# Optimization experiments

Measured on AMD Instinct MI355X. Metric: run time of the kernel, lower is better.

Reference implementation:

```python
import jax, jax.numpy as jnp
import numpy as np

B, N, C = 1, 2048, 1024
H, D = 16, 64          # num_heads, head_dim
S = 8                  # number of frames; tokens per frame = N // S
NEG_INF = jnp.float32(-1e30)  # stand-in for -inf, numerically safe under jit


def setup_inputs() -> dict:
    key = jax.random.key(0)
    ks = jax.random.split(key, 8)
    x = jax.random.normal(ks[0], (B, N, C), dtype=jnp.float32)
    # tokens grouped contiguously by frame (sorted frame ids)
    frame_ids = jnp.repeat(jnp.arange(S, dtype=jnp.int32), N // S)
    is_hub = jax.random.bernoulli(ks[1], 0.05, (N,))
    adj = jax.random.bernoulli(ks[2], 0.25, (S, S))
    adj = adj.at[jnp.arange(S), jnp.arange(S)].set(True)  # frames always see self
    frame_bias = jax.random.normal(ks[3], (S, S), dtype=jnp.float32) * 0.1
    Wqkv = jax.random.normal(ks[4], (C, 3 * C), dtype=jnp.float32) * 0.02
    bqkv = jnp.zeros((3 * C,), dtype=jnp.float32)
    Wproj = jax.random.normal(ks[5], (C, C), dtype=jnp.float32) * 0.02
    bproj = jnp.zeros((C,), dtype=jnp.float32)
    return {"x": x, "frame_ids": frame_ids, "is_hub": is_hub, "adj": adj,
            "frame_bias": frame_bias, "Wqkv": Wqkv, "bqkv": bqkv,
            "Wproj": Wproj, "bproj": bproj}


def reference(x, frame_ids, is_hub, adj, frame_bias, Wqkv, bqkv, Wproj, bproj):
    # qkv projection: (B,N,3C) -> (3,B,H,N,D)
    qkv = (x @ Wqkv + bqkv).reshape(B, N, 3, H, D).transpose(2, 0, 3, 1, 4)
    q, k, v = qkv[0], qkv[1], qkv[2]

    # flex_attention: scores scaled by 1/sqrt(D) BEFORE score_mod
    scores = jnp.einsum("bhnd,bhmd->bhnm", q, k) * (D ** -0.5)

    # score_mod, vectorized over all (qi,kj) pairs:
    fi = frame_ids                                   # (N,)
    allow = adj[fi][:, fi]                           # (N,N) frame adjacency per token pair
    diff_frame = fi[:, None] != fi[None, :]
    hub_block = diff_frame & (is_hub[:, None] | is_hub[None, :])
    allow = allow & ~hub_block                       # mask_hub_tokens=True
    bias = frame_bias[fi][:, fi]                     # soft_mask=True: add frame-level bias

    scores = jnp.where(allow, scores + bias, NEG_INF)  # broadcast over (b,h)
    attn = jax.nn.softmax(scores, axis=-1)
    out = jnp.einsum("bhnm,bhmd->bhnd", attn, v)
    out = out.transpose(0, 2, 1, 3).reshape(B, N, C)
    return out @ Wproj + bproj
```

## Files before the change

kernel.cpp:

```cpp
#include <hip/hip_runtime.h>

#define NTOK 2048
#define CDIM 1024
#define NHEAD 16
#define HDIM 64
#define NFRM 8
#define FTOK 256

typedef unsigned short ushort;
typedef unsigned long long u64;
typedef __attribute__((ext_vector_type(8))) short short8;
typedef __attribute__((ext_vector_type(8))) ushort ushort8;
typedef __attribute__((ext_vector_type(4))) ushort ushort4v;
typedef __attribute__((ext_vector_type(4))) float floatx4;

__device__ __forceinline__ ushort f2bf(float f) {
    unsigned int u = __float_as_uint(f);
    return (ushort)((u + 0x7fffu + ((u >> 16) & 1u)) >> 16);
}

__device__ __forceinline__ unsigned int cvt_pk_bf16(float lo, float hi) {
    unsigned int r;
    asm volatile("v_cvt_pk_bf16_f32 %0, %1, %2" : "=v"(r) : "v"(lo), "v"(hi));
    return r;
}

__device__ __forceinline__ void gload_lds16(const void* g, void* l) {
    __builtin_amdgcn_global_load_lds(
        (const __attribute__((address_space(1))) unsigned int*)(uintptr_t)g,
        (__attribute__((address_space(3))) unsigned int*)(unsigned int)(uintptr_t)l,
        16, 0, 0);
}

__global__ __launch_bounds__(256)
void prep_kernel(const float* __restrict__ x, ushort* __restrict__ xb,
                 const float* __restrict__ Wqkv, ushort* __restrict__ wqkvT,
                 const float* __restrict__ Wproj, ushort* __restrict__ wprojT,
                 const int* __restrict__ is_hub, u64* __restrict__ hubmask)
{
    __shared__ ushort LT[64][72];
    const int b = blockIdx.x, t = threadIdx.x;

    if (b < 2048) {
        int i = b * 256 + t;
        float4 f = ((const float4*)x)[i];
        ushort4v o = { f2bf(f.x), f2bf(f.y), f2bf(f.z), f2bf(f.w) };
        ((ushort4v*)xb)[i] = o;
        return;
    }
    if (b >= 3072) {
        if (t < NTOK / 64) {
            u64 m = 0;
            for (int j = 0; j < 64; ++j)
                m |= (u64)(is_hub[t * 64 + j] != 0) << j;
            hubmask[t] = m;
        }
        return;
    }

    const float* W; ushort* WT; int K, N, n0, k0;
    if (b < 2816) { int idx = b - 2048; W = Wqkv;  WT = wqkvT;  K = 1024; N = 3072;
                    n0 = (idx % 48) * 64; k0 = (idx / 48) * 64; }
    else          { int idx = b - 2816; W = Wproj; WT = wprojT; K = 1024; N = 1024;
                    n0 = (idx & 15) * 64; k0 = (idx >> 4) * 64; }

    const int kr = t >> 4, nc = t & 15;
#pragma unroll
    for (int i = 0; i < 4; ++i) {
        int k = kr + i * 16;
        float4 w4 = *(const float4*)(W + (size_t)(k0 + k) * N + n0 + nc * 4);
        LT[nc*4+0][k] = f2bf(w4.x);
        LT[nc*4+1][k] = f2bf(w4.y);
        LT[nc*4+2][k] = f2bf(w4.z);
        LT[nc*4+3][k] = f2bf(w4.w);
    }
    __syncthreads();
    const int n = t >> 2;
#pragma unroll
    for (int half = 0; half < 2; ++half) {
        int kc = (t & 3) + 4 * half;
        ushort8 v = *(const ushort8*)&LT[n][kc * 8];
        *(ushort8*)(WT + (size_t)(n0 + n) * K + k0 + kc * 8) = v;
    }
}

template<int BM>
__global__ __launch_bounds__(256)
void gemm_bt_kernel(const ushort* __restrict__ A, const ushort* __restrict__ BT,
                    const float* __restrict__ bias, void* __restrict__ out,
                    ushort* __restrict__ vtb,
                    int M, int N, int K, int mode)
{
    constexpr int MI = BM / 32;
    __shared__ ushort As[2][BM * 32];
    __shared__ ushort Bs[2][128 * 32];

    const int t = threadIdx.x;
    const int wave = t >> 6, lane = t & 63;
    const int quad = lane >> 4, l15 = lane & 15;
    const int row0 = blockIdx.y * BM, col0 = blockIdx.x * 128;
    const int wm = (wave >> 1) * (BM / 2), wn = (wave & 1) * 64;

    const int sr = lane >> 2;
    const int sc = (lane & 3) * 8;
    const int ra = wave * (BM / 4);
    const int rb = wave * 32;

    floatx4 acc[MI][4];
#pragma unroll
    for (int i = 0; i < MI; ++i)
#pragma unroll
        for (int j = 0; j < 4; ++j) acc[i][j] = (floatx4){0.f, 0.f, 0.f, 0.f};

#pragma unroll
    for (int ii = 0; ii < BM / 64; ++ii)
        gload_lds16(A + (size_t)(row0 + ra + ii * 16 + sr) * K + sc, &As[0][(ra + ii * 16) * 32]);
    gload_lds16(BT + (size_t)(col0 + rb      + sr) * K + sc, &Bs[0][ rb       * 32]);
    gload_lds16(BT + (size_t)(col0 + rb + 16 + sr) * K + sc, &Bs[0][(rb + 16) * 32]);

    const int nk = K >> 5;
    for (int ki = 0; ki < nk; ++ki) {
        __syncthreads();
        if (ki + 1 < nk) {
            const int kn = (ki + 1) << 5;
            const int b = (ki + 1) & 1;
#pragma unroll
            for (int ii = 0; ii < BM / 64; ++ii)
                gload_lds16(A + (size_t)(row0 + ra + ii * 16 + sr) * K + kn + sc, &As[b][(ra + ii * 16) * 32]);
            gload_lds16(BT + (size_t)(col0 + rb      + sr) * K + kn + sc, &Bs[b][ rb       * 32]);
            gload_lds16(BT + (size_t)(col0 + rb + 16 + sr) * K + kn + sc, &Bs[b][(rb + 16) * 32]);
        }
        const ushort* as = As[ki & 1];
        const ushort* bs = Bs[ki & 1];

        short8 af[MI], bfr[4];
#pragma unroll
        for (int i = 0; i < MI; ++i)
            af[i] = *(const short8*)&as[(wm + i * 16 + l15) * 32 + quad * 8];
#pragma unroll
        for (int j = 0; j < 4; ++j)
            bfr[j] = *(const short8*)&bs[(wn + j * 16 + l15) * 32 + quad * 8];
#pragma unroll
        for (int i = 0; i < MI; ++i)
#pragma unroll
            for (int j = 0; j < 4; ++j)
                acc[i][j] = __builtin_amdgcn_mfma_f32_16x16x32_bf16(af[i], bfr[j], acc[i][j], 0, 0, 0);
    }

    if (mode == 0) {
        float* outf = (float*)out;
#pragma unroll
        for (int j = 0; j < 4; ++j) {
            int col = col0 + wn + j * 16 + l15;
            float bb = bias[col];
#pragma unroll
            for (int i = 0; i < MI; ++i) {
                int rowb = row0 + wm + i * 16 + quad * 4;
#pragma unroll
                for (int r = 0; r < 4; ++r)
                    outf[(size_t)(rowb + r) * N + col] = acc[i][j][r] + bb;
            }
        }
    } else {
        ushort* outb = (ushort*)out;
#pragma unroll
        for (int j = 0; j < 4; ++j) {
            int col = col0 + wn + j * 16 + l15;
            float bb = bias[col];
            int part = col >> 10, hh = (col >> 6) & 15, d = col & 63;
            if (part < 2) {
                int half = d >> 5, qk = (d & 31) >> 3, elem = d & 7;
                ushort* base = outb + (size_t)(part * NHEAD + hh) * (NTOK * HDIM);
#pragma unroll
                for (int i = 0; i < MI; ++i) {
                    int rowb = row0 + wm + i * 16 + quad * 4;
#pragma unroll
                    for (int r = 0; r < 4; ++r) {
                        int tok = rowb + r;
                        int tile = tok >> 6, kk = tok & 63;
                        int nt = kk >> 4, lk = kk & 15;
                        base[(size_t)tile * 4096 + ((nt * 2 + half) * 64 + qk * 16 + lk) * 8 + elem]
                            = f2bf(acc[i][j][r] + bb);
                    }
                }
            } else {
                int dt = d >> 4, lv = d & 15;
                ushort* base = vtb + (size_t)hh * (NTOK * HDIM);
#pragma unroll
                for (int i = 0; i < MI; ++i) {
                    int rowb = row0 + wm + i * 16 + quad * 4;
                    int tile = rowb >> 6, kk = rowb & 63;
                    int bslot = ((kk & 15) << 2) | (kk >> 4);
#pragma unroll
                    for (int r = 0; r < 4; ++r) {
                        int s = bslot + 4 * r;
                        int off = ((dt * 2 + (s >> 5)) * 64 + ((s >> 3) & 3) * 16 + lv) * 8 + (s & 7);
                        base[(size_t)tile * 4096 + off] = f2bf(acc[i][j][r] + bb);
                    }
                }
            }
        }
    }
}

__global__ __launch_bounds__(512, 4)
void attn_tile_kernel(const ushort* __restrict__ qkvb,
                      const ushort* __restrict__ vTb,
                      const int* __restrict__ frame_ids,
                      const u64* __restrict__ hubmask,
                      const int* __restrict__ adj,
                      const float* __restrict__ frame_bias,
                      ushort* __restrict__ attnb)
{
    __shared__ ushort Ps[8][16 * 72];
    __shared__ float  Om[4][64][21];

    const int t = threadIdx.x;
    const int wave = t >> 6, lane = t & 63;
    const int wq = wave & 3, wk = wave >> 2;
    const int quad = lane >> 4, l15 = lane & 15;
    const int b = blockIdx.x;
    const int h = b & 15, q0 = (b >> 4) * 64;

    const ushort* Qh = qkvb + (size_t)h * (NTOK * HDIM);
    const ushort* Kh = qkvb + (size_t)(NHEAD + h) * (NTOK * HDIM);
    const ushort* Vh = vTb + (size_t)h * (NTOK * HDIM);

    const ushort* qt = Qh + (size_t)(q0 >> 6) * 4096;
    short8 aq0 = *(const short8*)(qt + ((wq * 2 + 0) * 64 + lane) * 8);
    short8 aq1 = *(const short8*)(qt + ((wq * 2 + 1) * 64 + lane) * 8);

    const int fq = frame_ids[q0];
    unsigned vpack = 0; int nv = 0;
#pragma unroll
    for (int f = 0; f < NFRM; ++f)
        if (adj[fq * NFRM + f]) { vpack |= (unsigned)f << (3 * nv); ++nv; }

    const u64 hmq = hubmask[q0 >> 6];
    int qh[4];
#pragma unroll
    for (int r = 0; r < 4; ++r) qh[r] = (int)((hmq >> (wq * 16 + quad * 4 + r)) & 1);

    float lpart[4] = {0.f, 0.f, 0.f, 0.f};
    floatx4 oacc[4];
#pragma unroll
    for (int dt = 0; dt < 4; ++dt) oacc[dt] = (floatx4){0.f, 0.f, 0.f, 0.f};

    const float C1 = 0.18033688011112042f;
    const float L2E = 1.4426950408889634f;

    const int nmine = nv * 2;
    int vt = wk;
    for (int j = 0; j < nmine; ++j, vt += 2) {
        const int fj = (int)((vpack >> (3 * (vt >> 2))) & 7u);
        const int k0 = fj * FTOK + (vt & 3) * 64;
        const float fbl = frame_bias[fq * NFRM + fj] * L2E;
        const bool same = (fj == fq);
        const u64 hmk = hubmask[k0 >> 6];

        const ushort* kt = Kh + (size_t)(k0 >> 6) * 4096;
        const ushort* vtp = Vh + (size_t)(k0 >> 6) * 4096;
        short8 kf[8], vf[8];
#pragma unroll
        for (int idx = 0; idx < 8; ++idx)
            kf[idx] = *(const short8*)(kt + (idx * 64 + lane) * 8);
#pragma unroll
        for (int idx = 0; idx < 8; ++idx)
            vf[idx] = *(const short8*)(vtp + (idx * 64 + lane) * 8);

        floatx4 s[4];
#pragma unroll
        for (int nt = 0; nt < 4; ++nt)
            s[nt] = (floatx4){0.f, 0.f, 0.f, 0.f};
        __builtin_amdgcn_s_setprio(1);
#pragma unroll
        for (int nt = 0; nt < 4; ++nt) {
            s[nt] = __builtin_amdgcn_mfma_f32_16x16x32_bf16(aq0, kf[2*nt],     s[nt], 0, 0, 0);
            s[nt] = __builtin_amdgcn_mfma_f32_16x16x32_bf16(aq1, kf[2*nt + 1], s[nt], 0, 0, 0);
        }
        __builtin_amdgcn_s_setprio(0);

        float mkf[4];
#pragma unroll
        for (int nt = 0; nt < 4; ++nt) {
            int kb = (int)(((unsigned)(hmk >> (nt * 16)) >> l15) & 1u);
            mkf[nt] = (same || !kb) ? 1.f : 0.f;
        }
        float mrf[4];
#pragma unroll
        for (int r = 0; r < 4; ++r) mrf[r] = (same || !qh[r]) ? 1.f : 0.f;

#pragma unroll
        for (int r = 0; r < 4; ++r) {
            float pv[4];
#pragma unroll
            for (int nt = 0; nt < 4; ++nt) {
                float e = __builtin_amdgcn_exp2f(fmaf(s[nt][r], C1, fbl));
                pv[nt] = e * mkf[nt] * mrf[r];
            }
            lpart[r] += (pv[0] + pv[1]) + (pv[2] + pv[3]);
            uint2 pk;
            pk.x = cvt_pk_bf16(pv[0], pv[1]);
            pk.y = cvt_pk_bf16(pv[2], pv[3]);
            *(uint2*)&Ps[wave][(quad * 4 + r) * 72 + l15 * 4] = pk;
        }

        short8 ap0 = *(const short8*)&Ps[wave][l15 * 72 + quad * 8];
        short8 ap1 = *(const short8*)&Ps[wave][l15 * 72 + 32 + quad * 8];
        __builtin_amdgcn_s_setprio(1);
#pragma unroll
        for (int dt = 0; dt < 4; ++dt) {
            oacc[dt] = __builtin_amdgcn_mfma_f32_16x16x32_bf16(ap0, vf[2*dt],     oacc[dt], 0, 0, 0);
            oacc[dt] = __builtin_amdgcn_mfma_f32_16x16x32_bf16(ap1, vf[2*dt + 1], oacc[dt], 0, 0, 0);
        }
        __builtin_amdgcn_s_setprio(0);
    }

    if (wk == 1) {
#pragma unroll
        for (int dt = 0; dt < 4; ++dt)
#pragma unroll
            for (int r = 0; r < 4; ++r) Om[wq][lane][dt * 4 + r] = oacc[dt][r];
#pragma unroll
        for (int r = 0; r < 4; ++r) Om[wq][lane][16 + r] = lpart[r];
    }
    __syncthreads();
    if (wk == 1) return;

#pragma unroll
    for (int dt = 0; dt < 4; ++dt)
#pragma unroll
        for (int r = 0; r < 4; ++r) oacc[dt][r] += Om[wq][lane][dt * 4 + r];
#pragma unroll
    for (int r = 0; r < 4; ++r) lpart[r] += Om[wq][lane][16 + r];

    float linv[4];
#pragma unroll
    for (int r = 0; r < 4; ++r) {
        float ls = lpart[r];
        ls += __shfl_xor(ls, 1);
        ls += __shfl_xor(ls, 2);
        ls += __shfl_xor(ls, 4);
        ls += __shfl_xor(ls, 8);
        linv[r] = 1.0f / ls;
    }

#pragma unroll
    for (int dt = 0; dt < 4; ++dt) {
        int col = h * HDIM + dt * 16 + l15;
#pragma unroll
        for (int r = 0; r < 4; ++r) {
            int row = q0 + wq * 16 + quad * 4 + r;
            attnb[(size_t)row * CDIM + col] = f2bf(oacc[dt][r] * linv[r]);
        }
    }
}

extern "C" void kernel_launch(void* const* d_in, const int* in_sizes, int n_in,
                              void* d_out, int out_size, void* d_ws, size_t ws_size,
                              hipStream_t stream)
{
    const float* x          = (const float*)d_in[0];
    const int*   frame_ids  = (const int*)d_in[1];
    const int*   is_hub     = (const int*)d_in[2];
    const int*   adj        = (const int*)d_in[3];
    const float* frame_bias = (const float*)d_in[4];
    const float* Wqkv       = (const float*)d_in[5];
    const float* bqkv       = (const float*)d_in[6];
    const float* Wproj      = (const float*)d_in[7];
    const float* bproj      = (const float*)d_in[8];
    float* out = (float*)d_out;

    ushort* xb     = (ushort*)d_ws;
    ushort* wqkvT  = xb     + 2097152;
    ushort* wprojT = wqkvT  + 3145728;
    ushort* qkvb   = wprojT + 1048576;
    ushort* vTb    = qkvb   + 6291456;
    ushort* attnb  = vTb    + 2097152;
    u64*    hubmask = (u64*)(attnb + 2097152);

    prep_kernel<<<dim3(3073), dim3(256), 0, stream>>>(
        x, xb, Wqkv, wqkvT, Wproj, wprojT, is_hub, hubmask);

    gemm_bt_kernel<128><<<dim3(3 * CDIM / 128, NTOK / 128), dim3(256), 0, stream>>>(
        xb, wqkvT, bqkv, qkvb, vTb, NTOK, 3 * CDIM, CDIM, 1);

    attn_tile_kernel<<<dim3(512), dim3(512), 0, stream>>>(
        qkvb, vTb, frame_ids, hubmask, adj, frame_bias, attnb);

    gemm_bt_kernel<64><<<dim3(CDIM / 128, NTOK / 64), dim3(256), 0, stream>>>(
        attnb, wprojT, bproj, out, nullptr, NTOK, CDIM, CDIM, 0);
}
```

Baseline: 141.9 us.

## Pre-swizzle A operand into MFMA fragment layout and load directly to registers

The bf16 activation matrices (converted x and the attention output) are now written in a tiled layout that matches the MFMA A-fragment, so the GEMM reads A straight from global memory into registers with register double-buffering instead of staging it through LDS. The B tile moves to a 64-wide K step with an XOR swizzle in LDS to avoid bank conflicts, and each sync now covers two MFMA K-substeps. This removes A-side LDS traffic and halves barrier count, at the cost of more register pressure and un-staged per-lane global loads for A.

After: 140.0 us (median of 2 runs). Within noise of the previous version (-1.3%).

```diff
diff --git a/kernel.cpp b/kernel.cpp
--- a/kernel.cpp
+++ b/kernel.cpp
@@ -31,6 +31,7 @@
         (__attribute__((address_space(3))) unsigned int*)(unsigned int)(uintptr_t)l,
         16, 0, 0);
 }
+
 
 __global__ __launch_bounds__(256)
 void prep_kernel(const float* __restrict__ x, ushort* __restrict__ xb,
@@ -43,9 +44,13 @@
 
     if (b < 2048) {
         int i = b * 256 + t;
+        int tok = i >> 8, c0 = (i & 255) * 4;
         float4 f = ((const float4*)x)[i];
         ushort4v o = { f2bf(f.x), f2bf(f.y), f2bf(f.z), f2bf(f.w) };
-        ((ushort4v*)xb)[i] = o;
+        size_t idx = ((size_t)((tok >> 6) * 32 + (c0 >> 5)) << 11)
+                   + ((((tok & 63) >> 4) * 4 + ((c0 >> 3) & 3)) << 7)
+                   + ((tok & 15) << 3) + (c0 & 7);
+        *(ushort4v*)&xb[idx] = o;
         return;
     }
     if (b >= 3072) {
@@ -86,14 +91,13 @@
 
 template<int BM>
 __global__ __launch_bounds__(256)
-void gemm_bt_kernel(const ushort* __restrict__ A, const ushort* __restrict__ BT,
+void gemm_bt_kernel(const ushort* __restrict__ Afrag, const ushort* __restrict__ BT,
                     const float* __restrict__ bias, void* __restrict__ out,
                     ushort* __restrict__ vtb,
                     int M, int N, int K, int mode)
 {
     constexpr int MI = BM / 32;
-    __shared__ ushort As[2][BM * 32];
-    __shared__ ushort Bs[2][128 * 32];
+    __shared__ ushort Bs[2][128 * 64];
 
     const int t = threadIdx.x;
     const int wave = t >> 6, lane = t & 63;
@@ -101,10 +105,14 @@
     const int row0 = blockIdx.y * BM, col0 = blockIdx.x * 128;
     const int wm = (wave >> 1) * (BM / 2), wn = (wave & 1) * 64;
 
-    const int sr = lane >> 2;
-    const int sc = (lane & 3) * 8;
-    const int ra = wave * (BM / 4);
     const int rb = wave * 32;
+    const int srb = lane >> 3;
+    const int scb = (((lane & 7) ^ (srb & 7)) << 3);
+
+    const int absRow = row0 + wm;
+    const int rowtile = absRow >> 6;
+    const int ibase = (absRow & 63) >> 4;
+    const ushort* Abase = Afrag + ((size_t)rowtile * 32 << 11) + lane * 8;
 
     floatx4 acc[MI][4];
 #pragma unroll
@@ -112,39 +120,56 @@
 #pragma unroll
         for (int j = 0; j < 4; ++j) acc[i][j] = (floatx4){0.f, 0.f, 0.f, 0.f};
 
-#pragma unroll
-    for (int ii = 0; ii < BM / 64; ++ii)
-        gload_lds16(A + (size_t)(row0 + ra + ii * 16 + sr) * K + sc, &As[0][(ra + ii * 16) * 32]);
-    gload_lds16(BT + (size_t)(col0 + rb      + sr) * K + sc, &Bs[0][ rb       * 32]);
-    gload_lds16(BT + (size_t)(col0 + rb + 16 + sr) * K + sc, &Bs[0][(rb + 16) * 32]);
-
-    const int nk = K >> 5;
-    for (int ki = 0; ki < nk; ++ki) {
+    const int NPH = K >> 6;
+    short8 a0[MI], a1[MI], an0[MI], an1[MI];
+
+#pragma unroll
+    for (int ii = 0; ii < 4; ++ii)
+        gload_lds16(BT + (size_t)(col0 + rb + ii * 8 + srb) * K + scb,
+                    &Bs[0][(rb + ii * 8) * 64]);
+#pragma unroll
+    for (int i = 0; i < MI; ++i) {
+        a0[i] = *(const short8*)(Abase + ((size_t)0 << 11) + ((ibase + i) << 9));
+        a1[i] = *(const short8*)(Abase + ((size_t)1 << 11) + ((ibase + i) << 9));
+    }
+
+    for (int p = 0; p < NPH; ++p) {
         __syncthreads();
-        if (ki + 1 < nk) {
-            const int kn = (ki + 1) << 5;
-            const int b = (ki + 1) & 1;
-#pragma unroll
-            for (int ii = 0; ii < BM / 64; ++ii)
-                gload_lds16(A + (size_t)(row0 + ra + ii * 16 + sr) * K + kn + sc, &As[b][(ra + ii * 16) * 32]);
-            gload_lds16(BT + (size_t)(col0 + rb      + sr) * K + kn + sc, &Bs[b][ rb       * 32]);
-            gload_lds16(BT + (size_t)(col0 + rb + 16 + sr) * K + kn + sc, &Bs[b][(rb + 16) * 32]);
-        }
-        const ushort* as = As[ki & 1];
-        const ushort* bs = Bs[ki & 1];
-
-        short8 af[MI], bfr[4];
+        if (p + 1 < NPH) {
+            const int nb = (p + 1) & 1;
+#pragma unroll
+            for (int ii = 0; ii < 4; ++ii)
+                gload_lds16(BT + (size_t)(col0 + rb + ii * 8 + srb) * K + (p + 1) * 64 + scb,
+                            &Bs[nb][(rb + ii * 8) * 64]);
+#pragma unroll
+            for (int i = 0; i < MI; ++i) {
+                an0[i] = *(const short8*)(Abase + ((size_t)(2 * p + 2) << 11) + ((ibase + i) << 9));
+                an1[i] = *(const short8*)(Abase + ((size_t)(2 * p + 3) << 11) + ((ibase + i) << 9));
+            }
+        }
+        const ushort* bs = Bs[p & 1];
+        const int swz = (l15 & 7) << 3;
+
+        short8 bfr[4];
+#pragma unroll
+        for (int j = 0; j < 4; ++j)
+            bfr[j] = *(const short8*)&bs[(((wn + j * 16 + l15) * 64) + quad * 8) ^ swz];
 #pragma unroll
         for (int i = 0; i < MI; ++i)
-            af[i] = *(const short8*)&as[(wm + i * 16 + l15) * 32 + quad * 8];
+#pragma unroll
+            for (int j = 0; j < 4; ++j)
+                acc[i][j] = __builtin_amdgcn_mfma_f32_16x16x32_bf16(a0[i], bfr[j], acc[i][j], 0, 0, 0);
 #pragma unroll
         for (int j = 0; j < 4; ++j)
-            bfr[j] = *(const short8*)&bs[(wn + j * 16 + l15) * 32 + quad * 8];
+            bfr[j] = *(const short8*)&bs[(((wn + j * 16 + l15) * 64) + 32 + quad * 8) ^ swz];
 #pragma unroll
         for (int i = 0; i < MI; ++i)
 #pragma unroll
             for (int j = 0; j < 4; ++j)
-                acc[i][j] = __builtin_amdgcn_mfma_f32_16x16x32_bf16(af[i], bfr[j], acc[i][j], 0, 0, 0);
+                acc[i][j] = __builtin_amdgcn_mfma_f32_16x16x32_bf16(a1[i], bfr[j], acc[i][j], 0, 0, 0);
+
+#pragma unroll
+        for (int i = 0; i < MI; ++i) { a0[i] = an0[i]; a1[i] = an1[i]; }
     }
 
     if (mode == 0) {
@@ -345,14 +370,15 @@
         linv[r] = 1.0f / ls;
     }
 
+    const size_t tbase = ((size_t)(q0 >> 6) * 32) << 11;
 #pragma unroll
     for (int dt = 0; dt < 4; ++dt) {
-        int col = h * HDIM + dt * 16 + l15;
-#pragma unroll
-        for (int r = 0; r < 4; ++r) {
-            int row = q0 + wq * 16 + quad * 4 + r;
-            attnb[(size_t)row * CDIM + col] = f2bf(oacc[dt][r] * linv[r]);
-        }
+        size_t kbase = tbase + ((size_t)(h * 2 + (dt >> 1)) << 11)
+                     + ((wq * 4 + (dt & 1) * 2 + (l15 >> 3)) << 7)
+                     + (quad << 5) + (l15 & 7);
+#pragma unroll
+        for (int r = 0; r < 4; ++r)
+            attnb[kbase + r * 8] = f2bf(oacc[dt][r] * linv[r]);
     }
 }
 
```
